# Performance work log

Measured on AMD Instinct MI355X. Metric: run time of the kernel, lower is better.

Reference implementation:

```python
import jax, jax.numpy as jnp
import numpy as np

D_MODEL, D_STATE, EXPAND = 1024, 16, 2
D_INNER = EXPAND * D_MODEL
BATCH, SEQ = 4, 4096


def setup_inputs() -> dict:
    key = jax.random.key(0)
    ks = jax.random.split(key, 9)
    s = 0.02
    return {
        "x": jax.random.normal(ks[0], (BATCH, SEQ, D_MODEL), jnp.float32),
        # torch Linear weight [out,in] stored transposed here as [in,out]
        "W_in": jax.random.normal(ks[1], (D_MODEL, 2 * D_INNER), jnp.float32) * s,
        "conv_w": jax.random.normal(ks[2], (D_INNER, 1, 3), jnp.float32) * s,  # depthwise, groups=D_INNER
        "conv_b": jax.random.normal(ks[3], (D_INNER,), jnp.float32) * s,
        "W_B": jax.random.normal(ks[4], (D_INNER, D_STATE), jnp.float32) * s,
        "W_C": jax.random.normal(ks[5], (D_INNER, D_STATE), jnp.float32) * s,
        "A": jax.random.normal(ks[6], (D_STATE,), jnp.float32),
        "D": jnp.ones((D_INNER,), jnp.float32),
        "W_out": jax.random.normal(ks[7], (D_INNER, D_MODEL), jnp.float32) * s,
    }


def reference(x, W_in, conv_w, conv_b, W_B, W_C, A, D, W_out):
    d_inner = conv_w.shape[0]
    # input projection and split into main / residual gate paths
    xr = jnp.einsum("bld,de->ble", x, W_in)  # [B, L, 2*d_inner]
    x_main, res = xr[..., :d_inner], xr[..., d_inner:]
    # depthwise conv1d along seq (kernel 3, pad 1)
    xc = jax.lax.conv_general_dilated(
        x_main.transpose(0, 2, 1), conv_w, (1,), [(1, 1)],
        dimension_numbers=("NCH", "OIH", "NCH"), feature_group_count=d_inner)
    xc = (xc + conv_b[None, :, None]).transpose(0, 2, 1)  # [B, L, d_inner]
    xc = jax.nn.silu(xc)
    # selective-scan inputs
    Bt = jnp.einsum("bli,is->bls", xc, W_B)  # [B, L, d_state]
    Ct = jnp.einsum("bli,is->bls", xc, W_C)
    decay = jnp.exp(-jax.nn.softplus(A))  # exp(A_diag), [d_state]

    def step(state, bc):
        b_t, c_t = bc
        state = state * decay + b_t  # i=0: zeros*decay + B[0] == B[0]
        return state, jnp.sum(state * c_t, axis=-1)  # scalar per batch

    _, ys = jax.lax.scan(step, jnp.zeros_like(Bt[:, 0]),
                         (Bt.transpose(1, 0, 2), Ct.transpose(1, 0, 2)))
    ys = ys.T  # [B, L]
    y = ys[..., None] + xc * D  # broadcast scan output across d_inner
    y = y * jax.nn.silu(res)
    return jnp.einsum("bli,id->bld", y, W_out)
```

## Files before the change

### kernel.cpp

```cpp
#include <hip/hip_runtime.h>


typedef _Float16 half8 __attribute__((ext_vector_type(8)));
typedef float floatx4 __attribute__((ext_vector_type(4)));

#define D_MODEL 1024
#define D_INNER 2048
#define SEQ     4096
#define NBATCH  4
#define NROWS   (NBATCH * SEQ)
#define CHUNK   16
#define NCHUNK  (SEQ / CHUNK)
#define NTASK   (NBATCH * NCHUNK)

__device__ __forceinline__ void async16(_Float16* lds, const _Float16* g) {
    __builtin_amdgcn_global_load_lds((const __attribute__((address_space(1))) void*)g,
                                     (__attribute__((address_space(3))) void*)lds, 16, 0, 0);
}

__device__ __forceinline__ float siluf(float x) {
    return x / (1.f + __expf(-x));
}

__device__ __forceinline__ float decay_of(const float* A, int s) {
    return __expf(-log1pf(__expf(A[s])));
}


__global__ __launch_bounds__(256) void convert_f32_f16(const float* __restrict__ src,
                                                       _Float16* __restrict__ dst) {
    size_t idx = ((size_t)blockIdx.x * 256 + threadIdx.x) * 8;
    float4 a = *(const float4*)(src + idx);
    float4 b = *(const float4*)(src + idx + 4);
    half8 o = {(_Float16)a.x, (_Float16)a.y, (_Float16)a.z, (_Float16)a.w,
               (_Float16)b.x, (_Float16)b.y, (_Float16)b.z, (_Float16)b.w};
    *(half8*)(dst + idx) = o;
}

__global__ __launch_bounds__(256) void transpose_to_f16(const float* __restrict__ src,
                                                        _Float16* __restrict__ dst,
                                                        int K, int N) {
    __shared__ float tile[32][33];
    int n0 = blockIdx.x * 32, k0 = blockIdx.y * 32;
    int x = threadIdx.x, y = threadIdx.y;
#pragma unroll
    for (int r = 0; r < 32; r += 8)
        tile[y + r][x] = src[(size_t)(k0 + y + r) * N + (n0 + x)];
    __syncthreads();
#pragma unroll
    for (int r = 0; r < 32; r += 8)
        dst[(size_t)(n0 + y + r) * K + (k0 + x)] = (_Float16)tile[x][y + r];
}

__global__ __launch_bounds__(256) void convert_wbct(const float* __restrict__ WB,
                                                    const float* __restrict__ WC,
                                                    _Float16* __restrict__ WBCT) {
    int idx = blockIdx.x * 256 + threadIdx.x;
    int n = idx >> 11, k = idx & 2047;
    float v = (n < 16) ? WB[k * 16 + n] : WC[k * 16 + (n - 16)];
    WBCT[idx] = (_Float16)v;
}


__device__ __forceinline__ void stage_half(const _Float16* __restrict__ src, int K,
                                           int rowBase, int k0, _Float16* ldsHalf) {
    const int tid = threadIdx.x;
    const int sr = tid >> 3, wid = tid >> 6;
    const int lc = ((tid & 7) ^ (sr & 7)) << 3;
#pragma unroll
    for (int r = 0; r < 2; r++) {
        const _Float16* g = src + (size_t)(rowBase + r * 64 + sr) * K + (k0 + lc);
        async16(ldsHalf + r * 4096 + wid * 512, g);
    }
}

__device__ __forceinline__ void loadA8(half8 af[4][2], const _Float16* Ab, int base,
                                       int sw0, int sw1) {
#pragma unroll
    for (int m = 0; m < 4; m++) {
        const _Float16* p = Ab + base + m * 1024;
        af[m][0] = *(const half8*)(p + sw0);
        af[m][1] = *(const half8*)(p + sw1);
    }
}

__device__ __forceinline__ void loadB4(half8 bf[2][2], const _Float16* Bb, int base,
                                       int sw0, int sw1) {
#pragma unroll
    for (int n = 0; n < 2; n++) {
        const _Float16* p = Bb + base + n * 1024;
        bf[n][0] = *(const half8*)(p + sw0);
        bf[n][1] = *(const half8*)(p + sw1);
    }
}

#define GP_MMA(MQ, NQ, BF)                                                              \
    __builtin_amdgcn_s_barrier();                                                       \
    __builtin_amdgcn_s_setprio(1);                                                      \
    _Pragma("unroll") for (int m = 0; m < 4; m++)                                       \
        _Pragma("unroll") for (int n = 0; n < 2; n++)                                   \
            _Pragma("unroll") for (int s = 0; s < 2; s++)                               \
                acc[(MQ) * 4 + m][(NQ) * 2 + n] = __builtin_amdgcn_mfma_f32_16x16x32_f16( \
                    af[m][s], (BF)[n][s], acc[(MQ) * 4 + m][(NQ) * 2 + n], 0, 0, 0);    \
    __builtin_amdgcn_s_setprio(0);                                                      \
    __builtin_amdgcn_s_barrier();

template <typename OutT>
__global__ __launch_bounds__(512, 2) void gemm256(const _Float16* __restrict__ A,
                                                  const _Float16* __restrict__ BT,
                                                  OutT* __restrict__ C,
                                                  int M, int N, int K) {
    __shared__ __align__(16) _Float16 smem[4 * 16384];
    _Float16* const AsBase = smem;
    _Float16* const BsBase = smem + 32768;

    const int tid = threadIdx.x;
    const int wid = tid >> 6, lane = tid & 63;
    const int wm = wid >> 2, wn = wid & 3;
    const int fr = lane & 15, q = lane >> 4, frq = fr & 7;
    const int sw0 = (q ^ frq) << 3;
    const int sw1 = ((4 + q) ^ frq) << 3;
    const int aB0 = (wm * 64 + fr) * 64;
    const int bB0 = (wn * 32 + fr) * 64;

    int lin = blockIdx.y * gridDim.x + blockIdx.x;
    const int nwg = gridDim.x * gridDim.y;
    lin = (lin & 7) * (nwg >> 3) + (lin >> 3);
    const int bx = lin % gridDim.x, by = lin / gridDim.x;
    const int row0 = by * 256, col0 = bx * 256;
    const int NT = K >> 6;

    floatx4 acc[8][4] = {};
    half8 af[4][2], bf0[2][2], bf1[2][2];

    stage_half(A,  K, row0,       0, AsBase);
    stage_half(BT, K, col0,       0, BsBase);
    stage_half(A,  K, row0 + 128, 0, AsBase + 8192);
    stage_half(BT, K, col0 + 128, 0, BsBase + 8192);
    if (NT > 1) {
        stage_half(A,  K, row0, 64, AsBase + 16384);
        stage_half(BT, K, col0, 64, BsBase + 16384);
        asm volatile("s_waitcnt vmcnt(4)" ::: "memory");
    } else {
        asm volatile("s_waitcnt vmcnt(0)" ::: "memory");
    }
    __builtin_amdgcn_s_barrier();
    loadB4(bf0, BsBase, bB0, sw0, sw1);

    for (int t = 0; t < NT; ++t) {
        _Float16* Ab  = AsBase + ((t & 1) << 14);
        _Float16* Bb  = BsBase + ((t & 1) << 14);
        _Float16* Abn = AsBase + (((t + 1) & 1) << 14);
        _Float16* Bbn = BsBase + (((t + 1) & 1) << 14);
        const int k1 = (t + 1) << 6, k2 = (t + 2) << 6;
        const bool s1 = (t + 1) < NT, s2 = (t + 2) < NT;

        loadA8(af, Ab, aB0, sw0, sw1);
        loadB4(bf1, Bb, bB0 + 8192, sw0, sw1);
        if (s1) stage_half(A, K, row0 + 128, k1, Abn + 8192);
        GP_MMA(0, 0, bf0);

        if (s1) stage_half(BT, K, col0 + 128, k1, Bbn + 8192);
        GP_MMA(0, 1, bf1);

        loadA8(af, Ab, aB0 + 8192, sw0, sw1);
        if (s2) stage_half(A, K, row0, k2, Ab);
        GP_MMA(1, 0, bf0);

        if (s2) stage_half(BT, K, col0, k2, Bb);
        if (s2) {
            asm volatile("s_waitcnt vmcnt(4)" ::: "memory");
        } else if (t + 2 == NT) {
            asm volatile("s_waitcnt vmcnt(0)" ::: "memory");
        }
        __builtin_amdgcn_s_barrier();
        loadB4(bf0, Bbn, bB0, sw0, sw1);
        GP_MMA(1, 1, bf1);
    }

    const int er = (lane >> 4) * 4, ec = lane & 15;
#pragma unroll
    for (int fi = 0; fi < 8; fi++)
#pragma unroll
        for (int fj = 0; fj < 4; fj++)
#pragma unroll
            for (int r = 0; r < 4; r++) {
                int row = row0 + (fi >> 2) * 128 + wm * 64 + (fi & 3) * 16 + er + r;
                int col = col0 + (fj >> 1) * 128 + wn * 32 + (fj & 1) * 16 + ec;
                C[(size_t)row * N + col] = (OutT)acc[fi][fj][r];
            }
}

__global__ __launch_bounds__(256) void conv_bc_fin(const _Float16* __restrict__ xr,
                                                   const float* __restrict__ cw,
                                                   const float* __restrict__ cb,
                                                   const _Float16* __restrict__ WBCT,
                                                   const float* __restrict__ A,
                                                   _Float16* __restrict__ xc,
                                                   float* __restrict__ BtCt,
                                                   float* __restrict__ fin) {
    __shared__ __align__(16) _Float16 As[4 * 32 * 128];
    const int tid = threadIdx.x, wid = tid >> 6, lane = tid & 63;
    const int row0 = blockIdx.x * 32;
    const int l0 = row0 & (SEQ - 1);
    const int cg = lane & 15;
    const int rg = lane >> 4;
    const int fr = lane & 15, q = lane >> 4;
    _Float16* As_w = As + wid * 4096;
    const int r0 = rg * 8;

    floatx4 acc[2][2] = {};

    for (int t = 0; t < 4; t++) {
        const int kbase = wid * 512 + t * 128;
        const int gcol = kbase + cg * 8;
        float w0[8], w1[8], w2[8], bb[8];
#pragma unroll
        for (int j = 0; j < 8; j++) {
            w0[j] = cw[(gcol + j) * 3];
            w1[j] = cw[(gcol + j) * 3 + 1];
            w2[j] = cw[(gcol + j) * 3 + 2];
            bb[j] = cb[gcol + j];
        }
        half8 prev = {}, cur, nxt;
        if (!(l0 == 0 && rg == 0))
            prev = *(const half8*)(xr + (size_t)(row0 + r0 - 1) * 4096 + gcol);
        cur = *(const half8*)(xr + (size_t)(row0 + r0) * 4096 + gcol);
#pragma unroll
        for (int r = 0; r < 8; r++) {
            if (r == 7 && rg == 3 && l0 + 32 == SEQ) {
                half8 z = {};
                nxt = z;
            } else {
                nxt = *(const half8*)(xr + (size_t)(row0 + r0 + r + 1) * 4096 + gcol);
            }
            half8 o;
#pragma unroll
            for (int j = 0; j < 8; j++) {
                float a = (float)prev[j] * w0[j] + (float)cur[j] * w1[j] +
                          (float)nxt[j] * w2[j] + bb[j];
                o[j] = (_Float16)siluf(a);
            }
            const int lrow = r0 + r;
            *(half8*)(xc + (size_t)(row0 + lrow) * D_INNER + gcol) = o;
            *(half8*)(As_w + lrow * 128 + ((cg ^ (lrow & 7)) * 8)) = o;
            prev = cur;
            cur = nxt;
        }
#pragma unroll
        for (int ks = 0; ks < 4; ks++) {
            half8 af[2], bf[2];
#pragma unroll
            for (int rt = 0; rt < 2; rt++)
                af[rt] = *(const half8*)(As_w + (rt * 16 + fr) * 128 +
                                         (((ks * 4 + q) ^ (fr & 7)) * 8));
#pragma unroll
            for (int ot = 0; ot < 2; ot++)
                bf[ot] = *(const half8*)(WBCT + (size_t)(ot * 16 + fr) * D_INNER +
                                         kbase + ks * 32 + q * 8);
#pragma unroll
            for (int rt = 0; rt < 2; rt++)
#pragma unroll
                for (int ot = 0; ot < 2; ot++)
                    acc[rt][ot] = __builtin_amdgcn_mfma_f32_16x16x32_f16(af[rt], bf[ot], acc[rt][ot], 0, 0, 0);
        }
    }

    __syncthreads();
    float* red = (float*)As;
    float* btl = (float*)As + 4096;
    const int er = (lane >> 4) * 4, ec = lane & 15;
#pragma unroll
    for (int rt = 0; rt < 2; rt++)
#pragma unroll
        for (int ot = 0; ot < 2; ot++)
#pragma unroll
            for (int rr = 0; rr < 4; rr++)
                red[wid * 1024 + (rt * 16 + er + rr) * 32 + ot * 16 + ec] = acc[rt][ot][rr];
    __syncthreads();
#pragma unroll
    for (int i = 0; i < 4; i++) {
        int idx = i * 256 + tid;
        float v = red[idx] + red[1024 + idx] + red[2048 + idx] + red[3072 + idx];
        btl[idx] = v;
        BtCt[(size_t)row0 * 32 + idx] = v;
    }
    __syncthreads();
    if (tid < 32) {
        const int ch = tid >> 4, s = tid & 15;
        const float decay = decay_of(A, s);
        float st = 0.f;
#pragma unroll
        for (int r = 0; r < CHUNK; r++)
            st = st * decay + btl[(ch * 16 + r) * 32 + s];
        fin[((row0 >> 4) + ch) * 16 + s] = st;
    }
}

__global__ __launch_bounds__(64) void scan_p2(const float* __restrict__ fin,
                                              const float* __restrict__ A,
                                              float* __restrict__ carry) {
    int t = threadIdx.x;
    int b = t >> 4, s = t & 15;
    float decay = decay_of(A, s);
    float d16 = decay;
#pragma unroll
    for (int k = 0; k < 4; k++) d16 *= d16;
    float cy = 0.f;
#pragma unroll 8
    for (int c = 0; c < NCHUNK; c++) {
        int idx = ((b * NCHUNK) + c) * 16 + s;
        carry[idx] = cy;
        cy = cy * d16 + fin[idx];
    }
}

__global__ __launch_bounds__(256) void scan_p3_fuse(const float* __restrict__ BtCt,
                                                    const float* __restrict__ A,
                                                    const float* __restrict__ carry,
                                                    const float* __restrict__ D,
                                                    const _Float16* __restrict__ xr,
                                                    _Float16* __restrict__ xc) {
    __shared__ float ysl[CHUNK];
    const int task = blockIdx.x;
    const int b = task >> 8, c = task & (NCHUNK - 1);
    const int row0 = b * SEQ + c * CHUNK;
    const int tid = threadIdx.x;

    if (tid < 16) {
        const int s = tid;
        const float decay = decay_of(A, s);
        size_t r = (size_t)row0 * 32;
        float bt[CHUNK], ct[CHUNK];
#pragma unroll
        for (int j = 0; j < CHUNK; j++) {
            bt[j] = BtCt[r + (size_t)j * 32 + s];
            ct[j] = BtCt[r + (size_t)j * 32 + 16 + s];
        }
        float st = carry[task * 16 + s];
        float yv[CHUNK];
#pragma unroll
        for (int j = 0; j < CHUNK; j++) {
            st = st * decay + bt[j];
            yv[j] = st * ct[j];
        }
#pragma unroll
        for (int j = 0; j < CHUNK; j++) {
            float y = yv[j];
            y += __shfl_xor(y, 1, 16);
            y += __shfl_xor(y, 2, 16);
            y += __shfl_xor(y, 4, 16);
            y += __shfl_xor(y, 8, 16);
            if (s == 0) ysl[j] = y;
        }
    }
    __syncthreads();

#pragma unroll
    for (int it = 0; it < 16; it++) {
        int chunk = it * 256 + tid;
        int rl = chunk >> 8;
        int colb = (chunk & 255) * 8;
        size_t row = (size_t)(row0 + rl);
        float yv = ysl[rl];
        half8 x8 = *(const half8*)(xc + row * D_INNER + colb);
        half8 r8 = *(const half8*)(xr + row * 4096 + 2048 + colb);
        float4 d0 = *(const float4*)(D + colb);
        float4 d1 = *(const float4*)(D + colb + 4);
        half8 o;
        float dd[8] = {d0.x, d0.y, d0.z, d0.w, d1.x, d1.y, d1.z, d1.w};
#pragma unroll
        for (int j = 0; j < 8; j++) {
            float y = yv + (float)x8[j] * dd[j];
            o[j] = (_Float16)(y * siluf((float)r8[j]));
        }
        *(half8*)(xc + row * D_INNER + colb) = o;
    }
}

extern "C" void kernel_launch(void* const* d_in, const int* in_sizes, int n_in,
                              void* d_out, int out_size, void* d_ws, size_t ws_size,
                              hipStream_t stream) {
    const float* x      = (const float*)d_in[0];
    const float* W_in   = (const float*)d_in[1];
    const float* conv_w = (const float*)d_in[2];
    const float* conv_b = (const float*)d_in[3];
    const float* W_B    = (const float*)d_in[4];
    const float* W_C    = (const float*)d_in[5];
    const float* A      = (const float*)d_in[6];
    const float* D      = (const float*)d_in[7];
    const float* W_out  = (const float*)d_in[8];
    float* out = (float*)d_out;

    char* ws = (char*)d_ws;
    size_t off = 0;
    auto alloc = [&](size_t bytes) { size_t o = off; off += (bytes + 255) & ~(size_t)255; return o; };
    _Float16* xh    = (_Float16*)(ws + alloc((size_t)NROWS * D_MODEL * 2));
    _Float16* WinT  = (_Float16*)(ws + alloc((size_t)4096 * 1024 * 2));
    _Float16* WoutT = (_Float16*)(ws + alloc((size_t)1024 * 2048 * 2));
    _Float16* WBCT  = (_Float16*)(ws + alloc((size_t)32 * 2048 * 2));
    _Float16* xr    = (_Float16*)(ws + alloc((size_t)NROWS * 4096 * 2));
    _Float16* xc    = (_Float16*)(ws + alloc((size_t)NROWS * D_INNER * 2));
    float*    BtCt  = (float*)(ws + alloc((size_t)NROWS * 32 * 4));
    float*    fin   = (float*)(ws + alloc((size_t)NTASK * 16 * 4));
    float*    carry = (float*)(ws + alloc((size_t)NTASK * 16 * 4));

    convert_f32_f16<<<(NROWS * D_MODEL) / (256 * 8), 256, 0, stream>>>(x, xh);
    transpose_to_f16<<<dim3(4096 / 32, 1024 / 32), dim3(32, 8), 0, stream>>>(W_in, WinT, 1024, 4096);
    transpose_to_f16<<<dim3(1024 / 32, 2048 / 32), dim3(32, 8), 0, stream>>>(W_out, WoutT, 2048, 1024);
    convert_wbct<<<(32 * 2048) / 256, 256, 0, stream>>>(W_B, W_C, WBCT);
    gemm256<_Float16><<<dim3(4096 / 256, NROWS / 256), 512, 0, stream>>>(xh, WinT, xr, NROWS, 4096, 1024);
    conv_bc_fin<<<NROWS / 32, 256, 0, stream>>>(xr, conv_w, conv_b, WBCT, A, xc, BtCt, fin);
    scan_p2<<<1, 64, 0, stream>>>(fin, A, carry);
    scan_p3_fuse<<<NTASK, 256, 0, stream>>>(BtCt, A, carry, D, xr, xc);
    gemm256<float><<<dim3(1024 / 256, NROWS / 256), 512, 0, stream>>>(xc, WoutT, out, NROWS, 1024, 2048);
}
```

Baseline: 437.0 us.

## Remap GEMM warps to 4x2 layout with 64x128 per-warp tiles and reordered staging

Changes the 8-warp arrangement in the 256x256 GEMM from 2x4 (two 64x32 subtiles per warp) to 4x2, so each warp owns one contiguous 64x128 tile. A fragments are loaded once per K-step and reused across four B column chunks, which cuts LDS reads of A, and the next step's A and B fragments are loaded early at the end of the previous iteration. The global-to-LDS staging order and vmcnt waits are reshuffled to match. Register pressure shifts toward B fragments, and the waitcnt and barrier ordering must stay correct.

```diff
diff --git a/kernel.cpp b/kernel.cpp
--- a/kernel.cpp
+++ b/kernel.cpp
@@ -74,34 +74,32 @@
     }
 }
 
-__device__ __forceinline__ void loadA8(half8 af[4][2], const _Float16* Ab, int base,
+__device__ __forceinline__ void loadA8(half8 af[4][2], const _Float16* p,
                                        int sw0, int sw1) {
 #pragma unroll
     for (int m = 0; m < 4; m++) {
-        const _Float16* p = Ab + base + m * 1024;
-        af[m][0] = *(const half8*)(p + sw0);
-        af[m][1] = *(const half8*)(p + sw1);
-    }
-}
-
-__device__ __forceinline__ void loadB4(half8 bf[2][2], const _Float16* Bb, int base,
+        af[m][0] = *(const half8*)(p + m * 1024 + sw0);
+        af[m][1] = *(const half8*)(p + m * 1024 + sw1);
+    }
+}
+
+__device__ __forceinline__ void loadB4(half8 bf[2][2], const _Float16* p,
                                        int sw0, int sw1) {
 #pragma unroll
     for (int n = 0; n < 2; n++) {
-        const _Float16* p = Bb + base + n * 1024;
-        bf[n][0] = *(const half8*)(p + sw0);
-        bf[n][1] = *(const half8*)(p + sw1);
-    }
-}
-
-#define GP_MMA(MQ, NQ, BF)                                                              \
+        bf[n][0] = *(const half8*)(p + n * 1024 + sw0);
+        bf[n][1] = *(const half8*)(p + n * 1024 + sw1);
+    }
+}
+
+#define GP_MMA(CB, BF)                                                                  \
     __builtin_amdgcn_s_barrier();                                                       \
     __builtin_amdgcn_s_setprio(1);                                                      \
     _Pragma("unroll") for (int m = 0; m < 4; m++)                                       \
         _Pragma("unroll") for (int n = 0; n < 2; n++)                                   \
             _Pragma("unroll") for (int s = 0; s < 2; s++)                               \
-                acc[(MQ) * 4 + m][(NQ) * 2 + n] = __builtin_amdgcn_mfma_f32_16x16x32_f16( \
-                    af[m][s], (BF)[n][s], acc[(MQ) * 4 + m][(NQ) * 2 + n], 0, 0, 0);    \
+                acc[m][(CB) * 2 + n] = __builtin_amdgcn_mfma_f32_16x16x32_f16(          \
+                    af[m][s], (BF)[n][s], acc[m][(CB) * 2 + n], 0, 0, 0);               \
     __builtin_amdgcn_s_setprio(0);                                                      \
     __builtin_amdgcn_s_barrier();
 
@@ -116,12 +114,12 @@
 
     const int tid = threadIdx.x;
     const int wid = tid >> 6, lane = tid & 63;
-    const int wm = wid >> 2, wn = wid & 3;
+    const int wm = wid >> 1, wn = wid & 1;
     const int fr = lane & 15, q = lane >> 4, frq = fr & 7;
     const int sw0 = (q ^ frq) << 3;
     const int sw1 = ((4 + q) ^ frq) << 3;
     const int aB0 = (wm * 64 + fr) * 64;
-    const int bB0 = (wn * 32 + fr) * 64;
+    const int bB0 = (wn * 128 + fr) * 64;
 
     int lin = blockIdx.y * gridDim.x + blockIdx.x;
     const int nwg = gridDim.x * gridDim.y;
@@ -130,22 +128,23 @@
     const int row0 = by * 256, col0 = bx * 256;
     const int NT = K >> 6;
 
-    floatx4 acc[8][4] = {};
-    half8 af[4][2], bf0[2][2], bf1[2][2];
+    floatx4 acc[4][8] = {};
+    half8 af[4][2], bfA[2][2], bfB[2][2];
 
     stage_half(A,  K, row0,       0, AsBase);
+    stage_half(A,  K, row0 + 128, 0, AsBase + 8192);
     stage_half(BT, K, col0,       0, BsBase);
-    stage_half(A,  K, row0 + 128, 0, AsBase + 8192);
     stage_half(BT, K, col0 + 128, 0, BsBase + 8192);
     if (NT > 1) {
-        stage_half(A,  K, row0, 64, AsBase + 16384);
-        stage_half(BT, K, col0, 64, BsBase + 16384);
-        asm volatile("s_waitcnt vmcnt(4)" ::: "memory");
+        stage_half(A, K, row0, 64, AsBase + 16384);
+        asm volatile("s_waitcnt vmcnt(2)" ::: "memory");
     } else {
         asm volatile("s_waitcnt vmcnt(0)" ::: "memory");
     }
     __builtin_amdgcn_s_barrier();
-    loadB4(bf0, BsBase, bB0, sw0, sw1);
+    asm volatile("" ::: "memory");
+    loadB4(bfA, BsBase + bB0, sw0, sw1);
+    loadA8(af, AsBase + aB0, sw0, sw1);
 
     for (int t = 0; t < NT; ++t) {
         _Float16* Ab  = AsBase + ((t & 1) << 14);
@@ -155,39 +154,53 @@
         const int k1 = (t + 1) << 6, k2 = (t + 2) << 6;
         const bool s1 = (t + 1) < NT, s2 = (t + 2) < NT;
 
-        loadA8(af, Ab, aB0, sw0, sw1);
-        loadB4(bf1, Bb, bB0 + 8192, sw0, sw1);
-        if (s1) stage_half(A, K, row0 + 128, k1, Abn + 8192);
-        GP_MMA(0, 0, bf0);
-
+        loadB4(bfB, Bb + bB0 + 2048, sw0, sw1);
+        if (s1) {
+            stage_half(A,  K, row0 + 128, k1, Abn + 8192);
+            stage_half(BT, K, col0,       k1, Bbn);
+        }
+        GP_MMA(0, bfA);
+
+        loadB4(bfA, Bb + bB0 + 4096, sw0, sw1);
         if (s1) stage_half(BT, K, col0 + 128, k1, Bbn + 8192);
-        GP_MMA(0, 1, bf1);
-
-        loadA8(af, Ab, aB0 + 8192, sw0, sw1);
+        GP_MMA(1, bfB);
+
+        loadB4(bfB, Bb + bB0 + 6144, sw0, sw1);
         if (s2) stage_half(A, K, row0, k2, Ab);
-        GP_MMA(1, 0, bf0);
-
-        if (s2) stage_half(BT, K, col0, k2, Bb);
+        GP_MMA(2, bfA);
+
         if (s2) {
-            asm volatile("s_waitcnt vmcnt(4)" ::: "memory");
-        } else if (t + 2 == NT) {
+            asm volatile("s_waitcnt vmcnt(2)" ::: "memory");
+        } else if (s1) {
             asm volatile("s_waitcnt vmcnt(0)" ::: "memory");
         }
         __builtin_amdgcn_s_barrier();
-        loadB4(bf0, Bbn, bB0, sw0, sw1);
-        GP_MMA(1, 1, bf1);
+        asm volatile("" ::: "memory");
+        if (s1) loadB4(bfA, Bbn + bB0, sw0, sw1);
+        __builtin_amdgcn_s_setprio(1);
+#pragma unroll
+        for (int m = 0; m < 4; m++)
+#pragma unroll
+            for (int n = 0; n < 2; n++)
+#pragma unroll
+                for (int s = 0; s < 2; s++)
+                    acc[m][6 + n] = __builtin_amdgcn_mfma_f32_16x16x32_f16(
+                        af[m][s], bfB[n][s], acc[m][6 + n], 0, 0, 0);
+        __builtin_amdgcn_s_setprio(0);
+        if (s1) loadA8(af, Abn + aB0, sw0, sw1);
+        __builtin_amdgcn_s_barrier();
     }
 
     const int er = (lane >> 4) * 4, ec = lane & 15;
 #pragma unroll
-    for (int fi = 0; fi < 8; fi++)
-#pragma unroll
-        for (int fj = 0; fj < 4; fj++)
+    for (int mi = 0; mi < 4; mi++)
+#pragma unroll
+        for (int cj = 0; cj < 8; cj++)
 #pragma unroll
             for (int r = 0; r < 4; r++) {
-                int row = row0 + (fi >> 2) * 128 + wm * 64 + (fi & 3) * 16 + er + r;
-                int col = col0 + (fj >> 1) * 128 + wn * 32 + (fj & 1) * 16 + ec;
-                C[(size_t)row * N + col] = (OutT)acc[fi][fj][r];
+                int row = row0 + wm * 64 + mi * 16 + er + r;
+                int col = col0 + wn * 128 + cj * 16 + ec;
+                C[(size_t)row * N + col] = (OutT)acc[mi][cj][r];
             }
 }
 
```

Result: slower. 448.9 us (+2.7%).
